# Performance work log

Hardware: AMD Instinct MI355X
Metric: run time of the kernel (lower is better)

## Reference

```python
import jax, jax.numpy as jnp
import numpy as np

J0 = 3
JBIG = 7
TH = 0.01
MM = 3.2 ** 2  # Gaussian window variance factor from get_phi


def get_phi(x):
    # phi(x) = sinc-like sin(pi x)/(pi x) * exp(-x^2/(2*mm)), with phi(0)=1
    t = jnp.pi * x
    t_safe = jnp.where(t == 0.0, 1.0, t)
    out = jnp.sin(t) * jnp.exp(-jnp.square(x) / (2.0 * MM)) / t_safe
    return jnp.where(t == 0.0, 1.0, out)


def nearest_idx(x, targets):
    # x: [N,1], targets: [K] -> index of nearest sample for each target, [K]
    return jnp.argmin(jnp.abs(x - targets[None, :]), axis=0)


def _outer_recon(wc, wr, C):
    # sum_{c,r} wc[:,c] wr[:,r] C[c,r]  (equivalent to the blockwise einsum +
    # tensordot over flattened (c,r) pairs in the torch code)
    return jnp.einsum('nc,cr,mr->nm', wc, C, wr)


def setup_inputs() -> dict:
    key = jax.random.key(0)
    k_img, k_xc, k_xr = jax.random.split(key, 3)
    N = 4096
    img = jax.random.normal(k_img, (N, N), dtype=jnp.float32)
    # sorted sample coordinates in [-1, 1] (domain spanned by wavelet translates)
    xc = jnp.sort(2.0 * jax.random.uniform(k_xc, (N, 1), dtype=jnp.float32) - 1.0, axis=0)
    xr = jnp.sort(2.0 * jax.random.uniform(k_xr, (N, 1), dtype=jnp.float32) - 1.0, axis=0)
    return {"img": img, "xc": xc, "xr": xr}


def reference(img, xc, xr):
    # ---- coarse approximation at scale j0 ----
    j0 = J0
    k = jnp.asarray(np.arange(-2 ** j0, 2 ** j0 + 1, 1), dtype=jnp.float32)  # [K0]
    phi_c = get_phi((2.0 ** j0) * xc - k[None, :])  # [N, K0]
    phi_r = get_phi((2.0 ** j0) * xr - k[None, :])  # [N, K0]
    xjk = k * (2.0 ** (-j0))
    ic = nearest_idx(xc, xjk)
    ir = nearest_idx(xr, xjk)
    F = img[ic[:, None], ir[None, :]]               # [K0, K0]
    approx = _outer_recon(phi_c, phi_r, F)          # [N, N]

    # ---- detail scales j0 .. J-1 ----
    for j in range(J0, JBIG):
        kj = jnp.asarray(np.arange((-2 ** (j + 1) - 1) / 2, 2 ** (j + 1) / 2, 0.5),
                         dtype=jnp.float32)          # [Kj] = 2^{j+2}+1
        xjk = (2.0 * kj + 1.0) * (2.0 ** (-j - 1))
        ic = nearest_idx(xc, xjk)
        ir = nearest_idx(xr, xjk)
        f = img[ic[:, None], ir[None, :]]            # [Kj, Kj]
        u = approx[ic[:, None], ir[None, :]]         # [Kj, Kj]
        diff = f - u
        # thresholded coefficient selection (torch.where -> mask, same math)
        D = jnp.where(jnp.abs(diff) > TH, diff, 0.0)
        psi_c = get_phi((2.0 ** (j + 1)) * xc - (2.0 * kj + 1.0)[None, :])  # [N, Kj]
        psi_r = get_phi((2.0 ** (j + 1)) * xr - (2.0 * kj + 1.0)[None, :])  # [N, Kj]
        approx = approx + _outer_recon(psi_c, psi_r, D)
    return approx
```

## Files before the change

kernel.cpp:

```cpp
#include <hip/hip_runtime.h>
#include <hip/hip_bf16.h>
#include <cstddef>
#include <cstdint>

#define NN 4096
#define KP 512
#define KTOT 501

typedef __attribute__((ext_vector_type(8))) short short8;
typedef __attribute__((ext_vector_type(4))) float f32x4;

#define GLB(p) ((const __attribute__((address_space(1))) void*)(p))
#define LDS(p) ((__attribute__((address_space(3))) void*)(p))

__device__ __forceinline__ float bf2f(unsigned short u) {
    union { unsigned int i; float f; } v; v.i = ((unsigned int)u) << 16; return v.f;
}

__device__ __forceinline__ void split_bf16(float v, unsigned short& h, unsigned short& l) {
    __hip_bfloat16 hb = __float2bfloat16(v);
    __hip_bfloat16 lb = __float2bfloat16(v - __bfloat162float(hb));
    h = *(unsigned short*)&hb;
    l = *(unsigned short*)&lb;
}

__device__ __forceinline__ float phi_eval(float x) {
    if (x == 0.0f) return 1.0f;
    const float PI_F = 3.14159265358979323846f;
    float rn = rintf(x);
    float r  = x - rn;
    float s  = __sinf(PI_F * r);
    if (((int)rn) & 1) s = -s;
    float e  = __expf(-x * x * (1.0f / 20.48f));
    return __fdividef(s * e, PI_F * x);
}

__device__ __forceinline__ void col_to_level(int col, int& l, int& off) {
    if      (col < 17)  { l = 0; off = 0;   }
    else if (col < 50)  { l = 1; off = 17;  }
    else if (col < 115) { l = 2; off = 50;  }
    else                { l = (col < 244) ? 3 : 4; off = (col < 244) ? 115 : 244; }
}

__global__ __launch_bounds__(256) void fused_pre(const float* __restrict__ xc,
                                                 const float* __restrict__ xr,
                                                 unsigned short* __restrict__ PCh,
                                                 unsigned short* __restrict__ PCl,
                                                 unsigned short* __restrict__ PRh,
                                                 unsigned short* __restrict__ PRl,
                                                 unsigned short* __restrict__ Ch,
                                                 int* __restrict__ idxAll) {
    __shared__ float sv[256];
    __shared__ int   si[256];
    const int b = blockIdx.x;
    const int tid = threadIdx.x;
    if (b < 2 * KTOT) {
        int side = (b >= KTOT);
        int col  = side ? b - KTOT : b;
        const float* x = side ? xr : xc;
        int l, off; col_to_level(col, l, off);
        int s = 8 << l;
        float target = (float)(col - off - s) / (float)s;
        float best = 1e30f; int bidx = 0;
        for (int n = tid; n < NN; n += 256) {
            float d = fabsf(x[n] - target);
            if (d < best) { best = d; bidx = n; }
        }
        sv[tid] = best; si[tid] = bidx;
        __syncthreads();
        for (int w = 128; w > 0; w >>= 1) {
            if (tid < w) {
                float ov = sv[tid + w]; int oi = si[tid + w];
                if (ov < sv[tid] || (ov == sv[tid] && oi < si[tid])) { sv[tid] = ov; si[tid] = oi; }
            }
            __syncthreads();
        }
        if (tid == 0) idxAll[b] = si[0];
    } else if (b < 2026) {
        const int i0 = (b - 1002) * 2048 + tid;
        #pragma unroll
        for (int j = 0; j < 8; ++j) {
            int i = i0 + j * 256;
            int n = i >> 9, col = i & 511;
            float pc = 0.f, pr = 0.f;
            if (col < KTOT) {
                int l, off; col_to_level(col, l, off);
                int s = 8 << l;
                float fo = (float)(col - off - s);
                float fs = (float)s;
                pc = phi_eval(fs * xc[n] - fo);
                pr = phi_eval(fs * xr[n] - fo);
            }
            unsigned short h, l2;
            split_bf16(pc, h, l2); PCh[i] = h; PCl[i] = l2;
            split_bf16(pr, h, l2); PRh[i] = h; PRl[i] = l2;
        }
    } else {
        uint4* z = (uint4*)Ch;
        const int g0 = (b - 2026) * 256 + tid;
        #pragma unroll
        for (int j = 0; j < 8; ++j) {
            int g = g0 + j * 8192;
            z[g] = make_uint4(0u, 0u, 0u, 0u);
        }
    }
}


template<int T, int OFF>
__global__ __launch_bounds__(256) void build_k(const float* __restrict__ img,
                                               const int* __restrict__ idxAll,
                                               const float* __restrict__ Usm,
                                               const unsigned short* __restrict__ PRh,
                                               const unsigned short* __restrict__ PRl,
                                               float* __restrict__ CdT,
                                               unsigned short* __restrict__ Ch,
                                               unsigned short* __restrict__ Cl) {
    int i = blockIdx.x * 256 + threadIdx.x;
    if (i >= T * T) return;
    int p = i / T, q = i - p * T;
    int ip = idxAll[OFF + p];
    int iq = idxAll[KTOT + OFF + q];
    float f = img[(size_t)ip * NN + iq];
    float val;
    if (OFF == 0) {
        val = f;
    } else {
        const float* u = Usm + (size_t)(OFF + p) * KP;
        const unsigned short* ph = PRh + (size_t)iq * KP;
        const unsigned short* pl = PRl + (size_t)iq * KP;
        float s0 = 0.f, s1 = 0.f, s2 = 0.f, s3 = 0.f;
        int k = 0;
        #pragma unroll 4
        for (; k + 4 <= OFF; k += 4) {
            ushort4 h4 = *(const ushort4*)(ph + k);
            ushort4 l4 = *(const ushort4*)(pl + k);
            float4  b4 = *(const float4*)(u + k);
            s0 += (bf2f(h4.x) + bf2f(l4.x)) * b4.x;
            s1 += (bf2f(h4.y) + bf2f(l4.y)) * b4.y;
            s2 += (bf2f(h4.z) + bf2f(l4.z)) * b4.z;
            s3 += (bf2f(h4.w) + bf2f(l4.w)) * b4.w;
        }
        float uu = (s0 + s1) + (s2 + s3);
        for (; k < OFF; ++k) uu += (bf2f(ph[k]) + bf2f(pl[k])) * u[k];
        float d = f - uu;
        val = (fabsf(d) > 0.01f) ? d : 0.0f;
    }
    size_t o = (size_t)(OFF + q) * KP + (OFF + p);
    CdT[o] = val;
    unsigned short h, l;
    split_bf16(val, h, l);
    Ch[o] = h; Cl[o] = l;
}

template<int T, int OFF>
__global__ __launch_bounds__(256) void update_k(const unsigned short* __restrict__ PCh,
                                                const unsigned short* __restrict__ PCl,
                                                const int* __restrict__ idxAll,
                                                const float* __restrict__ CdT,
                                                float* __restrict__ Usm) {
    int i = blockIdx.x * 256 + threadIdx.x;
    if (i >= KTOT * T) return;
    int r = i / T, t = i - r * T;
    const unsigned short* ah = PCh + (size_t)idxAll[r] * KP + OFF;
    const unsigned short* al = PCl + (size_t)idxAll[r] * KP + OFF;
    const float* b = CdT + (size_t)(OFF + t) * KP + OFF;
    constexpr int HEAD = (4 - (OFF & 3)) & 3;
    float s = 0.f;
    int k = 0;
    #pragma unroll
    for (; k < HEAD; ++k) s += (bf2f(ah[k]) + bf2f(al[k])) * b[k];
    float s0 = 0.f, s1 = 0.f, s2 = 0.f, s3 = 0.f;
    #pragma unroll 4
    for (; k + 4 <= T; k += 4) {
        ushort4 h4 = *(const ushort4*)(ah + k);
        ushort4 l4 = *(const ushort4*)(al + k);
        float4  b4 = *(const float4*)(b + k);
        s0 += (bf2f(h4.x) + bf2f(l4.x)) * b4.x;
        s1 += (bf2f(h4.y) + bf2f(l4.y)) * b4.y;
        s2 += (bf2f(h4.z) + bf2f(l4.z)) * b4.z;
        s3 += (bf2f(h4.w) + bf2f(l4.w)) * b4.w;
    }
    s += (s0 + s1) + (s2 + s3);
    for (; k < T; ++k) s += (bf2f(ah[k]) + bf2f(al[k])) * b[k];
    Usm[(size_t)r * KP + OFF + t] = s;
}

#define GEMM_BODY(Ahi_, Alo_, Bhi_, Blo_, XARR_, XBASE_, BMASK_)                       \
    __shared__ short As_h[128][32];                                                    \
    __shared__ short As_l[128][32];                                                    \
    __shared__ short Bs_h[128][32];                                                    \
    __shared__ short Bs_l[128][32];                                                    \
    const int tid  = threadIdx.x;                                                      \
    const int lane = tid & 63;                                                         \
    const int wave = tid >> 6;                                                         \
    const int wr   = wave >> 1;                                                        \
    const int wc   = wave & 1;                                                         \
    const int row0 = blockIdx.y * 128;                                                 \
    const int col0 = blockIdx.x * 128;                                                 \
    int list[16]; int nch = 0;                                                         \
    {                                                                                  \
        float xmn = XARR_[XBASE_];                                                     \
        float xmx = XARR_[(XBASE_) + 127];                                             \
        int mask = 0;                                                                  \
        const int off_[5] = {0, 17, 50, 115, 244};                                     \
        _Pragma("unroll")                                                              \
        for (int l = 0; l < 5; ++l) {                                                  \
            int s_ = 8 << l;                                                           \
            int clo = off_[l] + s_ + (int)floorf(s_ * xmn - 12.5f);                    \
            int chi = off_[l] + s_ + (int)ceilf (s_ * xmx + 12.5f);                    \
            if (clo < off_[l]) clo = off_[l];                                          \
            if (chi > off_[l] + 2 * s_) chi = off_[l] + 2 * s_;                        \
            for (int c = clo >> 5; c <= (chi >> 5); ++c) mask |= 1 << c;               \
        }                                                                              \
        mask &= (BMASK_);                                                              \
        for (int c = 0; c < 16; ++c) if ((mask >> c) & 1) list[nch++] = c;             \
    }                                                                                  \
    f32x4 acc[4][4];                                                                   \
    _Pragma("unroll")                                                                  \
    for (int i = 0; i < 4; ++i)                                                        \
        _Pragma("unroll")                                                              \
        for (int j = 0; j < 4; ++j) acc[i][j] = (f32x4){0.f, 0.f, 0.f, 0.f};           \
    const int srow = lane >> 2;                                                        \
    const int scol = (lane & 3) * 8;                                                   \
    for (int ic = 0; ic < nch; ++ic) {                                                 \
        const int k0 = list[ic] * 32;                                                  \
        _Pragma("unroll")                                                              \
        for (int s = 0; s < 2; ++s) {                                                  \
            const int rseg = wave * 32 + s * 16;                                       \
            const int r    = rseg + srow;                                              \
            const size_t ga = (size_t)(row0 + r) * KP + k0 + scol;                     \
            const size_t gb = (size_t)(col0 + r) * KP + k0 + scol;                     \
            __builtin_amdgcn_global_load_lds(GLB(Ahi_ + ga), LDS(&As_h[rseg][0]), 16, 0, 0); \
            __builtin_amdgcn_global_load_lds(GLB(Alo_ + ga), LDS(&As_l[rseg][0]), 16, 0, 0); \
            __builtin_amdgcn_global_load_lds(GLB(Bhi_ + gb), LDS(&Bs_h[rseg][0]), 16, 0, 0); \
            __builtin_amdgcn_global_load_lds(GLB(Blo_ + gb), LDS(&Bs_l[rseg][0]), 16, 0, 0); \
        }                                                                              \
        __syncthreads();                                                               \
        const int kb = (lane >> 4) * 8;                                                \
        short8 ah[4], al[4], bh[4], bl[4];                                             \
        _Pragma("unroll")                                                              \
        for (int mb = 0; mb < 4; ++mb) {                                               \
            const int rr = wr * 64 + mb * 16 + (lane & 15);                            \
            ah[mb] = *(const short8*)&As_h[rr][kb];                                    \
            al[mb] = *(const short8*)&As_l[rr][kb];                                    \
        }                                                                              \
        _Pragma("unroll")                                                              \
        for (int nb = 0; nb < 4; ++nb) {                                               \
            const int cc = wc * 64 + nb * 16 + (lane & 15);                            \
            bh[nb] = *(const short8*)&Bs_h[cc][kb];                                    \
            bl[nb] = *(const short8*)&Bs_l[cc][kb];                                    \
        }                                                                              \
        _Pragma("unroll")                                                              \
        for (int mb = 0; mb < 4; ++mb)                                                 \
            _Pragma("unroll")                                                          \
            for (int nb = 0; nb < 4; ++nb) {                                           \
                acc[mb][nb] = __builtin_amdgcn_mfma_f32_16x16x32_bf16(ah[mb], bh[nb], acc[mb][nb], 0, 0, 0); \
                acc[mb][nb] = __builtin_amdgcn_mfma_f32_16x16x32_bf16(ah[mb], bl[nb], acc[mb][nb], 0, 0, 0); \
                acc[mb][nb] = __builtin_amdgcn_mfma_f32_16x16x32_bf16(al[mb], bh[nb], acc[mb][nb], 0, 0, 0); \
            }                                                                          \
        __syncthreads();                                                               \
    }                                                                                  \
    const int orow = (lane >> 4) * 4;                                                  \
    const int ocol = lane & 15;

__global__ __launch_bounds__(256) void gemm_mfma_f32out(const short* __restrict__ Ahi,
                                                        const short* __restrict__ Alo,
                                                        const short* __restrict__ Bhi,
                                                        const short* __restrict__ Blo,
                                                        const float* __restrict__ xr,
                                                        float* __restrict__ out) {
    GEMM_BODY(Ahi, Alo, Bhi, Blo, xr, blockIdx.x * 128, 0xFFFF)
    #pragma unroll
    for (int mb = 0; mb < 4; ++mb)
        #pragma unroll
        for (int nb = 0; nb < 4; ++nb) {
            const int col = col0 + wc * 64 + nb * 16 + ocol;
            #pragma unroll
            for (int reg = 0; reg < 4; ++reg) {
                const int row = row0 + wr * 64 + mb * 16 + orow + reg;
                out[(size_t)row * NN + col] = acc[mb][nb][reg];
            }
        }
}

__global__ __launch_bounds__(256) void gemm_mfma_splitout(const short* __restrict__ Ahi,
                                                          const short* __restrict__ Alo,
                                                          const short* __restrict__ Bhi,
                                                          const short* __restrict__ Blo,
                                                          const float* __restrict__ xc,
                                                          unsigned short* __restrict__ Oh,
                                                          unsigned short* __restrict__ Ol) {
    const int bmask_tab[4] = {0x00FF, 0xFFF8, 0xFF80, 0xFF80};
    const int bm = bmask_tab[blockIdx.x];
    GEMM_BODY(Ahi, Alo, Bhi, Blo, xc, blockIdx.y * 128, bm)
    #pragma unroll
    for (int mb = 0; mb < 4; ++mb)
        #pragma unroll
        for (int nb = 0; nb < 4; ++nb) {
            const int col = col0 + wc * 64 + nb * 16 + ocol;
            #pragma unroll
            for (int reg = 0; reg < 4; ++reg) {
                const int row = row0 + wr * 64 + mb * 16 + orow + reg;
                unsigned short h, l;
                split_bf16(acc[mb][nb][reg], h, l);
                Oh[(size_t)row * KP + col] = h;
                Ol[(size_t)row * KP + col] = l;
            }
        }
}

extern "C" void kernel_launch(void* const* d_in, const int* in_sizes, int n_in,
                              void* d_out, int out_size, void* d_ws, size_t ws_size,
                              hipStream_t stream) {
    const float* img = (const float*)d_in[0];
    const float* xc  = (const float*)d_in[1];
    const float* xr  = (const float*)d_in[2];
    float* out = (float*)d_out;

    const size_t M2 = (size_t)NN * KP;
    unsigned short* PCh = (unsigned short*)d_ws;
    unsigned short* PCl = PCh + M2;
    unsigned short* PRh = PCl + M2;
    unsigned short* PRl = PRh + M2;
    unsigned short* Uh  = PRl + M2;
    unsigned short* Ul  = Uh + M2;
    float* Usm = (float*)(Ul + M2);
    float* CdT = Usm + (size_t)KP * KP;
    unsigned short* Ch = (unsigned short*)(CdT + (size_t)KP * KP);
    unsigned short* Cl = Ch + (size_t)KP * KP;
    int* idxAll = (int*)(Cl + (size_t)KP * KP);

    fused_pre<<<dim3(2058), 256, 0, stream>>>(xc, xr, PCh, PCl, PRh, PRl, Ch, idxAll);
    build_k<17, 0>   <<<dim3(2),   256, 0, stream>>>(img, idxAll, Usm, PRh, PRl, CdT, Ch, Cl);
    update_k<17, 0>  <<<dim3(34),  256, 0, stream>>>(PCh, PCl, idxAll, CdT, Usm);
    build_k<33, 17>  <<<dim3(5),   256, 0, stream>>>(img, idxAll, Usm, PRh, PRl, CdT, Ch, Cl);
    update_k<33, 17> <<<dim3(65),  256, 0, stream>>>(PCh, PCl, idxAll, CdT, Usm);
    build_k<65, 50>  <<<dim3(17),  256, 0, stream>>>(img, idxAll, Usm, PRh, PRl, CdT, Ch, Cl);
    update_k<65, 50> <<<dim3(128), 256, 0, stream>>>(PCh, PCl, idxAll, CdT, Usm);
    build_k<129, 115><<<dim3(66),  256, 0, stream>>>(img, idxAll, Usm, PRh, PRl, CdT, Ch, Cl);
    update_k<129, 115><<<dim3(253), 256, 0, stream>>>(PCh, PCl, idxAll, CdT, Usm);
    build_k<257, 244><<<dim3(259), 256, 0, stream>>>(img, idxAll, Usm, PRh, PRl, CdT, Ch, Cl);
    gemm_mfma_splitout<<<dim3(KP / 128, NN / 128), 256, 0, stream>>>(
        (const short*)PCh, (const short*)PCl, (const short*)Ch, (const short*)Cl, xc, Uh, Ul);
    gemm_mfma_f32out<<<dim3(NN / 128, NN / 128), 256, 0, stream>>>(
        (const short*)Uh, (const short*)Ul, (const short*)PRh, (const short*)PRl, xr, out);
}
```

Before: 227.1 us.

## Double-buffer LDS tiles and XOR-swizzle chunks in split-bf16 MFMA GEMM

The GEMM shared-memory tiles for the hi/lo A and B operands become two buffers, so the next k-chunk's global-to-LDS loads are issued while MFMAs run on the current chunk. This removes one barrier per iteration and is meant to hide global load latency behind compute. The 16-byte chunk positions in each LDS row are XOR-swizzled by row bits, on both the write and read side, to reduce LDS bank conflicts on the short8 fragment reads. In exchange, LDS use per block doubles, which can lower occupancy.

```diff
diff --git a/kernel.cpp b/kernel.cpp
--- a/kernel.cpp
+++ b/kernel.cpp
@@ -187,10 +187,10 @@
 }
 
 #define GEMM_BODY(Ahi_, Alo_, Bhi_, Blo_, XARR_, XBASE_, BMASK_)                       \
-    __shared__ short As_h[128][32];                                                    \
-    __shared__ short As_l[128][32];                                                    \
-    __shared__ short Bs_h[128][32];                                                    \
-    __shared__ short Bs_l[128][32];                                                    \
+    __shared__ short As_h[2][128][32];                                                 \
+    __shared__ short As_l[2][128][32];                                                 \
+    __shared__ short Bs_h[2][128][32];                                                 \
+    __shared__ short Bs_l[2][128][32];                                                 \
     const int tid  = threadIdx.x;                                                      \
     const int lane = tid & 63;                                                         \
     const int wave = tid >> 6;                                                         \
@@ -222,34 +222,37 @@
         _Pragma("unroll")                                                              \
         for (int j = 0; j < 4; ++j) acc[i][j] = (f32x4){0.f, 0.f, 0.f, 0.f};           \
     const int srow = lane >> 2;                                                        \
-    const int scol = (lane & 3) * 8;                                                   \
-    for (int ic = 0; ic < nch; ++ic) {                                                 \
-        const int k0 = list[ic] * 32;                                                  \
+    const int scol = ((lane & 3) ^ ((lane >> 3) & 3)) * 8;    \
+    auto stage_ = [&](int bb, int k0) {                                                \
         _Pragma("unroll")                                                              \
         for (int s = 0; s < 2; ++s) {                                                  \
             const int rseg = wave * 32 + s * 16;                                       \
-            const int r    = rseg + srow;                                              \
-            const size_t ga = (size_t)(row0 + r) * KP + k0 + scol;                     \
-            const size_t gb = (size_t)(col0 + r) * KP + k0 + scol;                     \
-            __builtin_amdgcn_global_load_lds(GLB(Ahi_ + ga), LDS(&As_h[rseg][0]), 16, 0, 0); \
-            __builtin_amdgcn_global_load_lds(GLB(Alo_ + ga), LDS(&As_l[rseg][0]), 16, 0, 0); \
-            __builtin_amdgcn_global_load_lds(GLB(Bhi_ + gb), LDS(&Bs_h[rseg][0]), 16, 0, 0); \
-            __builtin_amdgcn_global_load_lds(GLB(Blo_ + gb), LDS(&Bs_l[rseg][0]), 16, 0, 0); \
+            const size_t ga = (size_t)(row0 + rseg + srow) * KP + k0 + scol;           \
+            const size_t gb = (size_t)(col0 + rseg + srow) * KP + k0 + scol;           \
+            __builtin_amdgcn_global_load_lds(GLB(Ahi_ + ga), LDS(&As_h[bb][rseg][0]), 16, 0, 0); \
+            __builtin_amdgcn_global_load_lds(GLB(Alo_ + ga), LDS(&As_l[bb][rseg][0]), 16, 0, 0); \
+            __builtin_amdgcn_global_load_lds(GLB(Bhi_ + gb), LDS(&Bs_h[bb][rseg][0]), 16, 0, 0); \
+            __builtin_amdgcn_global_load_lds(GLB(Blo_ + gb), LDS(&Bs_l[bb][rseg][0]), 16, 0, 0); \
         }                                                                              \
-        __syncthreads();                                                               \
-        const int kb = (lane >> 4) * 8;                                                \
+    };                                                                                 \
+    const int kbsw = 8 * ((lane >> 4) ^ ((lane >> 1) & 3));    \
+    if (nch > 0) stage_(0, list[0] * 32);                                              \
+    __syncthreads();                                                                   \
+    for (int ic = 0; ic < nch; ++ic) {                                                 \
+        const int cb = ic & 1;                                                         \
+        if (ic + 1 < nch) stage_(cb ^ 1, list[ic + 1] * 32);                           \
         short8 ah[4], al[4], bh[4], bl[4];                                             \
         _Pragma("unroll")                                                              \
         for (int mb = 0; mb < 4; ++mb) {                                               \
             const int rr = wr * 64 + mb * 16 + (lane & 15);                            \
-            ah[mb] = *(const short8*)&As_h[rr][kb];                                    \
-            al[mb] = *(const short8*)&As_l[rr][kb];                                    \
+            ah[mb] = *(const short8*)&As_h[cb][rr][kbsw];                              \
+            al[mb] = *(const short8*)&As_l[cb][rr][kbsw];                              \
         }                                                                              \
         _Pragma("unroll")                                                              \
         for (int nb = 0; nb < 4; ++nb) {                                               \
             const int cc = wc * 64 + nb * 16 + (lane & 15);                            \
-            bh[nb] = *(const short8*)&Bs_h[cc][kb];                                    \
-            bl[nb] = *(const short8*)&Bs_l[cc][kb];                                    \
+            bh[nb] = *(const short8*)&Bs_h[cb][cc][kbsw];                              \
+            bl[nb] = *(const short8*)&Bs_l[cb][cc][kbsw];                              \
         }                                                                              \
         _Pragma("unroll")                                                              \
         for (int mb = 0; mb < 4; ++mb)                                                 \
```

Result: no change. 226.8 us (-0.1%).
